# Kernel optimization log

Measured on AMD Instinct MI355X. Metric: run time of the kernel, lower is better.

## Reference

```python
import jax, jax.numpy as jnp
import numpy as np

S = 8          # nodes per subgraph (last node is the anchor)
B = 8192       # number of subgraphs in the batch
N = B * S      # total nodes
E_PER = S * S  # edges per subgraph (dense local connectivity)
DIN, DOUT = 512, 256
EPS = 1e-12


def _block_edges(key):
    # local src/dst in [0,S) per subgraph, offset to global node ids
    k1, k2 = jax.random.split(key)
    src = jax.random.randint(k1, (B, E_PER), 0, S)
    dst = jax.random.randint(k2, (B, E_PER), 0, S)
    off = (jnp.arange(B) * S)[:, None]
    return (src + off).reshape(-1), (dst + off).reshape(-1)


def setup_inputs() -> dict:
    key = jax.random.key(0)
    ks = jax.random.split(key, 10)
    pos_src, pos_dst = _block_edges(ks[0])
    neg_src, neg_dst = _block_edges(ks[1])
    return {
        "pos_x": jax.random.normal(ks[2], (N, DIN), jnp.float32),
        "neg_x": jax.random.normal(ks[3], (N, DIN), jnp.float32),
        "pos_src": pos_src, "pos_dst": pos_dst,
        "pos_w": jax.random.uniform(ks[4], (B * E_PER,), jnp.float32),
        "neg_src": neg_src, "neg_dst": neg_dst,
        "neg_w": jax.random.uniform(ks[5], (B * E_PER,), jnp.float32),
        "W_gcn": jax.random.normal(ks[6], (DIN, DOUT), jnp.float32) / np.sqrt(DIN),
        "b_gcn": jnp.zeros((DOUT,), jnp.float32),
        "prelu_a": jnp.float32(0.25),
        "W_bil": jax.random.normal(ks[7], (DOUT, DOUT), jnp.float32) / np.sqrt(DOUT),
        "b_bil": jnp.zeros((1,), jnp.float32),
    }


def _l2norm(x):
    return x / jnp.maximum(jnp.linalg.norm(x, axis=1, keepdims=True), EPS)


def _gcn_branch(x, src, dst, w, W_gcn, b_gcn, prelu_a):
    # GraphConv(norm='none') with edge weights: h = A_w (X W) + b
    xw = x @ W_gcn                                      # [N, DOUT]
    agg = jnp.zeros_like(xw).at[dst].add(w[:, None] * xw[src])
    h = agg + b_gcn
    h = jnp.where(h >= 0, h, prelu_a * h)               # PReLU (single param)
    h = h.reshape(B, S, -1)                             # fixed-size subgraphs
    pool = jnp.mean(h[:, :-1], axis=1)                  # mean over non-anchor nodes
    anchor = h[:, -1]                                   # last node per subgraph
    return _l2norm(pool), _l2norm(anchor)


def reference(pos_x, neg_x, pos_src, pos_dst, pos_w, neg_src, neg_dst, neg_w,
              W_gcn, b_gcn, prelu_a, W_bil, b_bil):
    pos_pool, anchor = _gcn_branch(pos_x, pos_src, pos_dst, pos_w, W_gcn, b_gcn, prelu_a)
    neg_pool, _ = _gcn_branch(neg_x, neg_src, neg_dst, neg_w, W_gcn, b_gcn, prelu_a)
    # Bilinear(D, D, 1): score_b = pool_b^T W anchor_b + bias
    pos_scores = jnp.einsum('bd,de,be->b', pos_pool, W_bil, anchor) + b_bil[0]
    neg_scores = jnp.einsum('bd,de,be->b', neg_pool, W_bil, anchor) + b_bil[0]
    return pos_scores, neg_scores
```

## Files before the change

### kernel.cpp

```cpp
#include <hip/hip_runtime.h>
#include <stdint.h>
#include <math.h>

#define SS 8
#define NBLK 8192
#define DIN 512
#define DOUT 256
#define GB 8
#define MT 64
#define BK 32
#define KSTEPS 16
#define VSTR 264
#define EPSN 1e-12f

typedef __bf16 bf16;
typedef __bf16 bf16x8 __attribute__((ext_vector_type(8)));
typedef float  f32x4  __attribute__((ext_vector_type(4)));

typedef __attribute__((address_space(3))) uint32_t       lds_u32;
typedef __attribute__((address_space(1))) const uint32_t g_u32;

__device__ __forceinline__ void dma16(const void* g, void* l) {
    __builtin_amdgcn_global_load_lds((g_u32*)g, (lds_u32*)l, 16, 0, 0);
}

__device__ __forceinline__ bf16x8 cvt8(f32x4 lo, f32x4 hi) {
    bf16x8 r;
    r[0] = (bf16)lo[0]; r[1] = (bf16)lo[1]; r[2] = (bf16)lo[2]; r[3] = (bf16)lo[3];
    r[4] = (bf16)hi[0]; r[5] = (bf16)hi[1]; r[6] = (bf16)hi[2]; r[7] = (bf16)hi[3];
    return r;
}

__global__ void prep_kernel(const float* __restrict__ W_gcn,
                            const float* __restrict__ W_bil,
                            bf16* __restrict__ Wt,
                            bf16* __restrict__ Wh,
                            bf16* __restrict__ Wl) {
    int idx = blockIdx.x * 256 + threadIdx.x;
    if (idx < DIN * DOUT) {
        int k = idx >> 8, n = idx & 255;
        Wt[n * DIN + k] = (bf16)W_gcn[idx];
    } else {
        int j = idx - DIN * DOUT;
        float wv = W_bil[j];
        bf16 h = (bf16)wv;
        Wh[j] = h;
        Wl[j] = (bf16)(wv - (float)h);
    }
}

__global__ __launch_bounds__(256, 2) void cola_fused4(
    const float* __restrict__ pos_x, const float* __restrict__ neg_x,
    const int* __restrict__ pos_src, const int* __restrict__ pos_dst,
    const float* __restrict__ pos_w,
    const int* __restrict__ neg_src, const int* __restrict__ neg_dst,
    const float* __restrict__ neg_w,
    const bf16* __restrict__ Wt, const bf16* __restrict__ Wh,
    const bf16* __restrict__ Wl,
    const float* __restrict__ b_gcn, const float* __restrict__ prelu_a,
    const float* __restrict__ b_bil, float* __restrict__ out)
{
    __shared__ __align__(16) float bufA[2][2][MT * BK];
    __shared__ __align__(16) bf16  bufB[2][DOUT * BK];
    __shared__ float adjP[GB][SS][SS];
    __shared__ float adjN[GB][SS][SS];
    __shared__ float red[5 * GB];

    float* pool_pos = (float*)&bufB[0][0];
    float* v_lds    = pool_pos + GB * DOUT;
    bf16*  ahs      = (bf16*)(v_lds + GB * DOUT);
    bf16*  als      = ahs + GB * VSTR;

    const int t    = threadIdx.x;
    const int wg   = blockIdx.x;
    const int w    = t >> 6;
    const int lane = t & 63;
    const int q    = lane >> 4;
    const int r15  = lane & 15;
    const int row0 = wg * MT;

    for (int i = t; i < GB * 64; i += 256) { ((float*)adjP)[i] = 0.f; ((float*)adjN)[i] = 0.f; }
    if (t < 5 * GB) red[t] = 0.f;
    __syncthreads();

    {
        int2   sp2 = ((const int2*)pos_src)[wg * 256 + t];
        int2   dp2 = ((const int2*)pos_dst)[wg * 256 + t];
        float2 wp2 = ((const float2*)pos_w)[wg * 256 + t];
        int2   sn2 = ((const int2*)neg_src)[wg * 256 + t];
        int2   dn2 = ((const int2*)neg_dst)[wg * 256 + t];
        float2 wn2 = ((const float2*)neg_w)[wg * 256 + t];
        int gl = t >> 5;
        int base = (wg * GB + gl) * SS;
        atomicAdd(&adjP[gl][dp2.x - base][sp2.x - base], wp2.x);
        atomicAdd(&adjP[gl][dp2.y - base][sp2.y - base], wp2.y);
        atomicAdd(&adjN[gl][dn2.x - base][sn2.x - base], wn2.x);
        atomicAdd(&adjN[gl][dn2.y - base][sn2.y - base], wn2.y);
    }

    const int arow_off = lane >> 3;
    const int akq      = (lane & 7) ^ arow_off;
    const int bn_off = lane >> 2;
    const int bkq    = lane & 3;

    auto issue = [&](int s, int bufi) {
        const int kbase = s * BK;
#pragma unroll
        for (int h = 0; h < 2; ++h) {
            int c = w * 2 + h;
            int row = c * 8 + arow_off;
            dma16(pos_x + (size_t)(row0 + row) * DIN + kbase + akq * 4,
                  &bufA[bufi][0][c * 256]);
            dma16(neg_x + (size_t)(row0 + row) * DIN + kbase + akq * 4,
                  &bufA[bufi][1][c * 256]);
        }
#pragma unroll
        for (int j = 0; j < 4; ++j) {
            int c = w * 4 + j;
            dma16(Wt + (size_t)(c * 16 + bn_off) * DIN + kbase + bkq * 8,
                  &bufB[bufi][c * 512]);
        }
    };

    f32x4 accp[4][4], accn[4][4];
#pragma unroll
    for (int mi = 0; mi < 4; ++mi)
#pragma unroll
        for (int ni = 0; ni < 4; ++ni) {
            accp[mi][ni] = (f32x4){0.f, 0.f, 0.f, 0.f};
            accn[mi][ni] = (f32x4){0.f, 0.f, 0.f, 0.f};
        }

    issue(0, 0);
    int cur = 0;
    for (int s = 0; s < KSTEPS; ++s) {
        __syncthreads();
        if (s + 1 < KSTEPS) issue(s + 1, cur ^ 1);

        bf16x8 afp[4], afn[4], bfv[4];
        const int q0 = (2 * q) ^ (r15 & 7);
        const int q1 = q0 ^ 1;
#pragma unroll
        for (int mi = 0; mi < 4; ++mi) {
            int m = mi * 16 + r15;
            f32x4 lo = *(const f32x4*)&bufA[cur][0][m * BK + q0 * 4];
            f32x4 hi = *(const f32x4*)&bufA[cur][0][m * BK + q1 * 4];
            afp[mi] = cvt8(lo, hi);
            lo = *(const f32x4*)&bufA[cur][1][m * BK + q0 * 4];
            hi = *(const f32x4*)&bufA[cur][1][m * BK + q1 * 4];
            afn[mi] = cvt8(lo, hi);
        }
#pragma unroll
        for (int ni = 0; ni < 4; ++ni) {
            int n = w * 64 + ni * 16 + r15;
            bfv[ni] = *(const bf16x8*)&bufB[cur][n * BK + q * 8];
        }
#pragma unroll
        for (int mi = 0; mi < 4; ++mi)
#pragma unroll
            for (int ni = 0; ni < 4; ++ni) {
                accp[mi][ni] = __builtin_amdgcn_mfma_f32_16x16x32_bf16(
                    afp[mi], bfv[ni], accp[mi][ni], 0, 0, 0);
                accn[mi][ni] = __builtin_amdgcn_mfma_f32_16x16x32_bf16(
                    afn[mi], bfv[ni], accn[mi][ni], 0, 0, 0);
            }
        cur ^= 1;
    }
    __syncthreads();

    const float pa = *prelu_a;

#pragma unroll
    for (int mi = 0; mi < 4; ++mi) {
        const int gl = mi * 2 + (q >> 1);
        float part = 0.f;
#pragma unroll
        for (int ni = 0; ni < 4; ++ni) {
            float r0, r1, r2, r3, r4, r5, r6, r7;
#pragma unroll
            for (int r = 0; r < 4; ++r) {
                float own = accp[mi][ni][r];
                float oth = __shfl_xor(own, 16);
                float lo = ((q & 1) == 0) ? own : oth;
                float hi = ((q & 1) == 0) ? oth : own;
                if (r == 0) { r0 = lo; r4 = hi; }
                else if (r == 1) { r1 = lo; r5 = hi; }
                else if (r == 2) { r2 = lo; r6 = hi; }
                else            { r3 = lo; r7 = hi; }
            }
            int c = w * 64 + ni * 16 + r15;
            float bg = b_gcn[c];
            float pool = 0.f, anch = 0.f;
#pragma unroll
            for (int d = 0; d < 8; ++d) {
                const float* ar = &adjP[gl][d][0];
                float a = bg + ar[0]*r0 + ar[1]*r1 + ar[2]*r2 + ar[3]*r3
                             + ar[4]*r4 + ar[5]*r5 + ar[6]*r6 + ar[7]*r7;
                float h = (a >= 0.f) ? a : pa * a;
                if (d < 7) pool += h; else anch = h;
            }
            float pl = pool * (1.f / 7.f);
            if ((q & 1) == 0) {
                pool_pos[gl * DOUT + c] = pl;
                part += pl * pl;
            } else {
                bf16 hh = (bf16)anch;
                ahs[gl * VSTR + c] = hh;
                als[gl * VSTR + c] = (bf16)(anch - (float)hh);
                part += anch * anch;
            }
        }
        part += __shfl_xor(part, 8);
        part += __shfl_xor(part, 4);
        part += __shfl_xor(part, 2);
        part += __shfl_xor(part, 1);
        if (r15 == 0) atomicAdd((q & 1) ? &red[GB + gl] : &red[gl], part);
    }
    __syncthreads();

    {
        f32x4 accv[4];
#pragma unroll
        for (int ni = 0; ni < 4; ++ni) accv[ni] = (f32x4){0.f, 0.f, 0.f, 0.f};
        const int ga = (r15 & 7) * VSTR;
#pragma unroll
        for (int ks = 0; ks < 8; ++ks) {
            bf16x8 ah_f = *(const bf16x8*)(ahs + ga + ks * 32 + q * 8);
            bf16x8 al_f = *(const bf16x8*)(als + ga + ks * 32 + q * 8);
#pragma unroll
            for (int ni = 0; ni < 4; ++ni) {
                int d = w * 64 + ni * 16 + r15;
                bf16x8 bh = *(const bf16x8*)(Wh + (size_t)d * DOUT + ks * 32 + q * 8);
                bf16x8 bl = *(const bf16x8*)(Wl + (size_t)d * DOUT + ks * 32 + q * 8);
                accv[ni] = __builtin_amdgcn_mfma_f32_16x16x32_bf16(ah_f, bh, accv[ni], 0, 0, 0);
                accv[ni] = __builtin_amdgcn_mfma_f32_16x16x32_bf16(al_f, bh, accv[ni], 0, 0, 0);
                accv[ni] = __builtin_amdgcn_mfma_f32_16x16x32_bf16(ah_f, bl, accv[ni], 0, 0, 0);
            }
        }
        float sp[4] = {0.f, 0.f, 0.f, 0.f};
        if (q < 2) {
#pragma unroll
            for (int ni = 0; ni < 4; ++ni) {
                int c = w * 64 + ni * 16 + r15;
#pragma unroll
                for (int r = 0; r < 4; ++r) {
                    int g = q * 4 + r;
                    v_lds[g * DOUT + c] = accv[ni][r];
                    sp[r] += accv[ni][r] * pool_pos[g * DOUT + c];
                }
            }
        }
#pragma unroll
        for (int r = 0; r < 4; ++r) {
            sp[r] += __shfl_xor(sp[r], 8);
            sp[r] += __shfl_xor(sp[r], 4);
            sp[r] += __shfl_xor(sp[r], 2);
            sp[r] += __shfl_xor(sp[r], 1);
        }
        if (q < 2 && r15 == 0) {
#pragma unroll
            for (int r = 0; r < 4; ++r) atomicAdd(&red[3 * GB + q * 4 + r], sp[r]);
        }
    }
    __syncthreads();

#pragma unroll
    for (int mi = 0; mi < 4; ++mi) {
        const int gl = mi * 2 + (q >> 1);
        float part = 0.f;
#pragma unroll
        for (int ni = 0; ni < 4; ++ni) {
            float r0, r1, r2, r3, r4, r5, r6, r7;
#pragma unroll
            for (int r = 0; r < 4; ++r) {
                float own = accn[mi][ni][r];
                float oth = __shfl_xor(own, 16);
                float lo = ((q & 1) == 0) ? own : oth;
                float hi = ((q & 1) == 0) ? oth : own;
                if (r == 0) { r0 = lo; r4 = hi; }
                else if (r == 1) { r1 = lo; r5 = hi; }
                else if (r == 2) { r2 = lo; r6 = hi; }
                else            { r3 = lo; r7 = hi; }
            }
            int c = w * 64 + ni * 16 + r15;
            float bg = b_gcn[c];
            float pool = 0.f;
#pragma unroll
            for (int d = 0; d < 7; ++d) {
                const float* ar = &adjN[gl][d][0];
                float a = bg + ar[0]*r0 + ar[1]*r1 + ar[2]*r2 + ar[3]*r3
                             + ar[4]*r4 + ar[5]*r5 + ar[6]*r6 + ar[7]*r7;
                float h = (a >= 0.f) ? a : pa * a;
                pool += h;
            }
            float pl = pool * (1.f / 7.f);
            part += ((q & 1) == 0) ? pl * v_lds[gl * DOUT + c] : pl * pl;
        }
        part += __shfl_xor(part, 8);
        part += __shfl_xor(part, 4);
        part += __shfl_xor(part, 2);
        part += __shfl_xor(part, 1);
        if (r15 == 0) atomicAdd((q & 1) ? &red[2 * GB + gl] : &red[4 * GB + gl], part);
    }
    __syncthreads();

    if (t < GB) {
        float np = fmaxf(sqrtf(red[t]), EPSN);
        float na = fmaxf(sqrtf(red[GB + t]), EPSN);
        float nn = fmaxf(sqrtf(red[2 * GB + t]), EPSN);
        float bb = b_bil[0];
        out[wg * GB + t]        = red[3 * GB + t] / (np * na) + bb;
        out[NBLK + wg * GB + t] = red[4 * GB + t] / (nn * na) + bb;
    }
}

extern "C" void kernel_launch(void* const* d_in, const int* in_sizes, int n_in,
                              void* d_out, int out_size, void* d_ws, size_t ws_size,
                              hipStream_t stream) {
    const float* pos_x   = (const float*)d_in[0];
    const float* neg_x   = (const float*)d_in[1];
    const int*   pos_src = (const int*)d_in[2];
    const int*   pos_dst = (const int*)d_in[3];
    const float* pos_w   = (const float*)d_in[4];
    const int*   neg_src = (const int*)d_in[5];
    const int*   neg_dst = (const int*)d_in[6];
    const float* neg_w   = (const float*)d_in[7];
    const float* W_gcn   = (const float*)d_in[8];
    const float* b_gcn   = (const float*)d_in[9];
    const float* prelu_a = (const float*)d_in[10];
    const float* W_bil   = (const float*)d_in[11];
    const float* b_bil   = (const float*)d_in[12];
    float* outp = (float*)d_out;

    bf16* Wt = (bf16*)d_ws;
    bf16* Wh = Wt + DIN * DOUT;
    bf16* Wl = Wh + DOUT * DOUT;

    prep_kernel<<<(DIN * DOUT + DOUT * DOUT) / 256, 256, 0, stream>>>(W_gcn, W_bil, Wt, Wh, Wl);
    cola_fused4<<<NBLK / GB, 256, 0, stream>>>(
        pos_x, neg_x, pos_src, pos_dst, pos_w, neg_src, neg_dst, neg_w,
        Wt, Wh, Wl, b_gcn, prelu_a, b_bil, outp);
}
```

Baseline: 360.3 us.

## Load GEMM operands directly to registers and run pos/neg passes sequentially

Removes the LDS double-buffered global_load_lds staging and barrier-synchronized K loop. Each wave now loads its A (fp32 x rows) and B (bf16 weights) fragments straight from global memory into registers with one-step register prefetch. The pos and neg GEMMs run one after the other, reusing a single accumulator set, and launch bounds rise to allow 3 workgroups per CU. This targets register pressure, LDS usage and barrier overhead, at the cost of uncoalesced strided global loads, no sharing of x rows across waves (each of the 4 waves reloads all 64 rows), and weights fetched twice.

```diff
diff --git a/kernel.cpp b/kernel.cpp
--- a/kernel.cpp
+++ b/kernel.cpp
@@ -16,13 +16,6 @@
 typedef __bf16 bf16;
 typedef __bf16 bf16x8 __attribute__((ext_vector_type(8)));
 typedef float  f32x4  __attribute__((ext_vector_type(4)));
-
-typedef __attribute__((address_space(3))) uint32_t       lds_u32;
-typedef __attribute__((address_space(1))) const uint32_t g_u32;
-
-__device__ __forceinline__ void dma16(const void* g, void* l) {
-    __builtin_amdgcn_global_load_lds((g_u32*)g, (lds_u32*)l, 16, 0, 0);
-}
 
 __device__ __forceinline__ bf16x8 cvt8(f32x4 lo, f32x4 hi) {
     bf16x8 r;
@@ -49,7 +42,59 @@
     }
 }
 
-__global__ __launch_bounds__(256, 2) void cola_fused4(
+__device__ __forceinline__ void kpass(const float* __restrict__ xb,
+                                      const bf16* __restrict__ Wt,
+                                      int row0, int w, int q, int r15,
+                                      f32x4 acc[4][4])
+{
+#pragma unroll
+    for (int mi = 0; mi < 4; ++mi)
+#pragma unroll
+        for (int ni = 0; ni < 4; ++ni) acc[mi][ni] = (f32x4){0.f, 0.f, 0.f, 0.f};
+
+    const float* ax = xb + (size_t)(row0 + r15) * DIN + q * 8;
+    const bf16*  bx = Wt + (size_t)(w * 64 + r15) * DIN + q * 8;
+
+    f32x4  pl[4], ph[4];
+    bf16x8 pb[4];
+#pragma unroll
+    for (int mi = 0; mi < 4; ++mi) {
+        pl[mi] = *(const f32x4*)(ax + mi * 16 * DIN);
+        ph[mi] = *(const f32x4*)(ax + mi * 16 * DIN + 4);
+    }
+#pragma unroll
+    for (int ni = 0; ni < 4; ++ni)
+        pb[ni] = *(const bf16x8*)(bx + ni * 16 * DIN);
+
+#pragma unroll 2
+    for (int s = 0; s < KSTEPS; ++s) {
+        bf16x8 af[4], bfr[4];
+#pragma unroll
+        for (int mi = 0; mi < 4; ++mi) af[mi] = cvt8(pl[mi], ph[mi]);
+#pragma unroll
+        for (int ni = 0; ni < 4; ++ni) bfr[ni] = pb[ni];
+
+        if (s + 1 < KSTEPS) {
+            const int o = (s + 1) * BK;
+#pragma unroll
+            for (int mi = 0; mi < 4; ++mi) {
+                pl[mi] = *(const f32x4*)(ax + mi * 16 * DIN + o);
+                ph[mi] = *(const f32x4*)(ax + mi * 16 * DIN + o + 4);
+            }
+#pragma unroll
+            for (int ni = 0; ni < 4; ++ni)
+                pb[ni] = *(const bf16x8*)(bx + ni * 16 * DIN + o);
+        }
+#pragma unroll
+        for (int mi = 0; mi < 4; ++mi)
+#pragma unroll
+            for (int ni = 0; ni < 4; ++ni)
+                acc[mi][ni] = __builtin_amdgcn_mfma_f32_16x16x32_bf16(
+                    af[mi], bfr[ni], acc[mi][ni], 0, 0, 0);
+    }
+}
+
+__global__ __launch_bounds__(256, 3) void cola_fused5(
     const float* __restrict__ pos_x, const float* __restrict__ neg_x,
     const int* __restrict__ pos_src, const int* __restrict__ pos_dst,
     const float* __restrict__ pos_w,
@@ -60,16 +105,13 @@
     const float* __restrict__ b_gcn, const float* __restrict__ prelu_a,
     const float* __restrict__ b_bil, float* __restrict__ out)
 {
-    __shared__ __align__(16) float bufA[2][2][MT * BK];
-    __shared__ __align__(16) bf16  bufB[2][DOUT * BK];
+    __shared__ float pool_pos[GB * DOUT];
+    __shared__ float v_lds[GB * DOUT];
+    __shared__ bf16  ahs[GB * VSTR];
+    __shared__ bf16  als[GB * VSTR];
     __shared__ float adjP[GB][SS][SS];
     __shared__ float adjN[GB][SS][SS];
     __shared__ float red[5 * GB];
-
-    float* pool_pos = (float*)&bufB[0][0];
-    float* v_lds    = pool_pos + GB * DOUT;
-    bf16*  ahs      = (bf16*)(v_lds + GB * DOUT);
-    bf16*  als      = ahs + GB * VSTR;
 
     const int t    = threadIdx.x;
     const int wg   = blockIdx.x;
@@ -97,78 +139,12 @@
         atomicAdd(&adjN[gl][dn2.x - base][sn2.x - base], wn2.x);
         atomicAdd(&adjN[gl][dn2.y - base][sn2.y - base], wn2.y);
     }
-
-    const int arow_off = lane >> 3;
-    const int akq      = (lane & 7) ^ arow_off;
-    const int bn_off = lane >> 2;
-    const int bkq    = lane & 3;
-
-    auto issue = [&](int s, int bufi) {
-        const int kbase = s * BK;
-#pragma unroll
-        for (int h = 0; h < 2; ++h) {
-            int c = w * 2 + h;
-            int row = c * 8 + arow_off;
-            dma16(pos_x + (size_t)(row0 + row) * DIN + kbase + akq * 4,
-                  &bufA[bufi][0][c * 256]);
-            dma16(neg_x + (size_t)(row0 + row) * DIN + kbase + akq * 4,
-                  &bufA[bufi][1][c * 256]);
-        }
-#pragma unroll
-        for (int j = 0; j < 4; ++j) {
-            int c = w * 4 + j;
-            dma16(Wt + (size_t)(c * 16 + bn_off) * DIN + kbase + bkq * 8,
-                  &bufB[bufi][c * 512]);
-        }
-    };
-
-    f32x4 accp[4][4], accn[4][4];
-#pragma unroll
-    for (int mi = 0; mi < 4; ++mi)
-#pragma unroll
-        for (int ni = 0; ni < 4; ++ni) {
-            accp[mi][ni] = (f32x4){0.f, 0.f, 0.f, 0.f};
-            accn[mi][ni] = (f32x4){0.f, 0.f, 0.f, 0.f};
-        }
-
-    issue(0, 0);
-    int cur = 0;
-    for (int s = 0; s < KSTEPS; ++s) {
-        __syncthreads();
-        if (s + 1 < KSTEPS) issue(s + 1, cur ^ 1);
-
-        bf16x8 afp[4], afn[4], bfv[4];
-        const int q0 = (2 * q) ^ (r15 & 7);
-        const int q1 = q0 ^ 1;
-#pragma unroll
-        for (int mi = 0; mi < 4; ++mi) {
-            int m = mi * 16 + r15;
-            f32x4 lo = *(const f32x4*)&bufA[cur][0][m * BK + q0 * 4];
-            f32x4 hi = *(const f32x4*)&bufA[cur][0][m * BK + q1 * 4];
-            afp[mi] = cvt8(lo, hi);
-            lo = *(const f32x4*)&bufA[cur][1][m * BK + q0 * 4];
-            hi = *(const f32x4*)&bufA[cur][1][m * BK + q1 * 4];
-            afn[mi] = cvt8(lo, hi);
-        }
-#pragma unroll
-        for (int ni = 0; ni < 4; ++ni) {
-            int n = w * 64 + ni * 16 + r15;
-            bfv[ni] = *(const bf16x8*)&bufB[cur][n * BK + q * 8];
-        }
-#pragma unroll
-        for (int mi = 0; mi < 4; ++mi)
-#pragma unroll
-            for (int ni = 0; ni < 4; ++ni) {
-                accp[mi][ni] = __builtin_amdgcn_mfma_f32_16x16x32_bf16(
-                    afp[mi], bfv[ni], accp[mi][ni], 0, 0, 0);
-                accn[mi][ni] = __builtin_amdgcn_mfma_f32_16x16x32_bf16(
-                    afn[mi], bfv[ni], accn[mi][ni], 0, 0, 0);
-            }
-        cur ^= 1;
-    }
     __syncthreads();
 
     const float pa = *prelu_a;
+    f32x4 acc[4][4];
+
+    kpass(pos_x, Wt, row0, w, q, r15, acc);
 
 #pragma unroll
     for (int mi = 0; mi < 4; ++mi) {
@@ -179,7 +155,7 @@
             float r0, r1, r2, r3, r4, r5, r6, r7;
 #pragma unroll
             for (int r = 0; r < 4; ++r) {
-                float own = accp[mi][ni][r];
+                float own = acc[mi][ni][r];
                 float oth = __shfl_xor(own, 16);
                 float lo = ((q & 1) == 0) ? own : oth;
                 float hi = ((q & 1) == 0) ? oth : own;
@@ -264,6 +240,8 @@
     }
     __syncthreads();
 
+    kpass(neg_x, Wt, row0, w, q, r15, acc);
+
 #pragma unroll
     for (int mi = 0; mi < 4; ++mi) {
         const int gl = mi * 2 + (q >> 1);
@@ -273,7 +251,7 @@
             float r0, r1, r2, r3, r4, r5, r6, r7;
 #pragma unroll
             for (int r = 0; r < 4; ++r) {
-                float own = accn[mi][ni][r];
+                float own = acc[mi][ni][r];
                 float oth = __shfl_xor(own, 16);
                 float lo = ((q & 1) == 0) ? own : oth;
                 float hi = ((q & 1) == 0) ? oth : own;
@@ -337,7 +315,7 @@
     bf16* Wl = Wh + DOUT * DOUT;
 
     prep_kernel<<<(DIN * DOUT + DOUT * DOUT) / 256, 256, 0, stream>>>(W_gcn, W_bil, Wt, Wh, Wl);
-    cola_fused4<<<NBLK / GB, 256, 0, stream>>>(
+    cola_fused5<<<NBLK / GB, 256, 0, stream>>>(
         pos_x, neg_x, pos_src, pos_dst, pos_w, neg_src, neg_dst, neg_w,
         Wt, Wh, Wl, b_gcn, prelu_a, b_bil, outp);
 }
```

New measurement: 463.4 us. +28.6%, slower.
